# Performance work log

Hardware: AMD Instinct MI355X
Metric: run time of the kernel (lower is better)

The kernel has to match this reference:

```python
import jax, jax.numpy as jnp
import numpy as np
import math

N, E_EDGES, G = 25000, 400000, 128
D_NODE, D_EDGE, D_PE = 64, 16, 16
H_DIM, N_HEADS, N_LAYERS = 128, 8, 4
D_HEAD = H_DIM // N_HEADS
BN_EPS = 1e-5
SCALE = 1.0 / math.sqrt(D_HEAD)


def _bn(x, gamma, beta):
    # BatchNorm1d with batch statistics (training-mode math), biased variance
    mu = x.mean(0)
    var = x.var(0)
    return (x - mu) * jax.lax.rsqrt(var + BN_EPS) * gamma + beta


def _seg_softmax(score, seg, n):
    # softmax over edges sharing the same destination node (PyG softmax semantics)
    m = jax.lax.stop_gradient(jax.ops.segment_max(score, seg, num_segments=n))
    ex = jnp.exp(score - m[seg])
    den = jax.ops.segment_sum(ex, seg, num_segments=n)
    return ex / (den[seg] + 1e-16)


def _mlp(x, W1, b1, W2, b2):
    return jax.nn.relu(x @ W1 + b1) @ W2 + b2


def _forward(x, edge_attr, pe, Wn, We, Wpe, Wqkv, bqkv, WEl, bEl, WOl, bOl, WOel, bOel,
             fW1, fb1, fW2, fb2, feW1, feb1, feW2, feb2, bng, bnb,
             muW1, mub1, muW2, mub2, lvW1, lvb1, lvW2, lvb2, edge_index, batch):
    src, dst = edge_index[0], edge_index[1]  # messages flow src(j) -> dst(i)
    h = x @ Wn + pe @ Wpe                    # [N, H_DIM]
    e = edge_attr @ We                       # [E, H_DIM]
    for l in range(N_LAYERS):
        Q = (h @ Wqkv[l, 0] + bqkv[l, 0]).reshape(-1, N_HEADS, D_HEAD)
        K = (h @ Wqkv[l, 1] + bqkv[l, 1]).reshape(-1, N_HEADS, D_HEAD)
        V = (h @ Wqkv[l, 2] + bqkv[l, 2]).reshape(-1, N_HEADS, D_HEAD)
        Eh = (e @ WEl[l] + bEl[l]).reshape(-1, N_HEADS, D_HEAD)
        qijk = Eh * (Q[dst] * K[src]) * SCALE            # [E, H, Dh] edge-modulated scores
        alpha = _seg_softmax(qijk.sum(-1), dst, N)       # [E, H]
        agg = jax.ops.segment_sum(alpha[..., None] * V[src], dst, num_segments=N)
        agg = agg.reshape(-1, H_DIM)                     # [N, H_DIM] ('sum' aggregator)
        # node branch: WO + residual, BN, FFN, residual, BN
        hn = _bn(agg @ WOl[l] + bOl[l] + h, bng[l, 0], bnb[l, 0])
        hn = _bn(hn + _mlp(hn, fW1[l], fb1[l], fW2[l], fb2[l]), bng[l, 1], bnb[l, 1])
        # edge branch: pre-softmax scores are the edge update
        en = _bn(qijk.reshape(-1, H_DIM) @ WOel[l] + bOel[l] + e, bng[l, 2], bnb[l, 2])
        en = _bn(en + _mlp(en, feW1[l], feb1[l], feW2[l], feb2[l]), bng[l, 3], bnb[l, 3])
        h, e = hn, en
    g = jax.ops.segment_sum(h, batch, num_segments=G)    # [G, H_DIM] global 'sum' pool
    mu = _mlp(g, muW1, mub1, muW2, mub2)
    log_var = _mlp(g, lvW1, lvb1, lvW2, lvb2)
    return mu, jnp.exp(0.5 * log_var)                    # eval branch: (mu, std)


def setup_inputs() -> dict:
    key = jax.random.key(0)
    ks = iter(jax.random.split(key, 40))
    def nrm(shape, scale=1.0):
        return jax.random.normal(next(ks), shape, jnp.float32) * scale
    s = lambda fan: 1.0 / math.sqrt(fan)
    L = N_LAYERS
    d = {}
    d['x'] = nrm((N, D_NODE))
    d['edge_attr'] = nrm((E_EDGES, D_EDGE))
    d['pe'] = nrm((N, D_PE))
    d['edge_index'] = jax.random.randint(next(ks), (2, E_EDGES), 0, N, jnp.int32)
    d['batch'] = jnp.sort(jax.random.randint(next(ks), (N,), 0, G, jnp.int32))
    d['Wn'] = nrm((D_NODE, H_DIM), s(D_NODE))
    d['We'] = nrm((D_EDGE, H_DIM), s(D_EDGE))
    d['Wpe'] = nrm((D_PE, H_DIM), s(D_PE))
    d['Wqkv'] = nrm((L, 3, H_DIM, H_DIM), s(H_DIM)); d['bqkv'] = jnp.zeros((L, 3, H_DIM))
    d['WEl'] = nrm((L, H_DIM, H_DIM), s(H_DIM)); d['bEl'] = jnp.zeros((L, H_DIM))
    d['WOl'] = nrm((L, H_DIM, H_DIM), s(H_DIM)); d['bOl'] = jnp.zeros((L, H_DIM))
    d['WOel'] = nrm((L, H_DIM, H_DIM), s(H_DIM)); d['bOel'] = jnp.zeros((L, H_DIM))
    for p in ['f', 'fe']:
        d[p + 'W1'] = nrm((L, H_DIM, H_DIM), s(H_DIM)); d[p + 'b1'] = jnp.zeros((L, H_DIM))
        d[p + 'W2'] = nrm((L, H_DIM, H_DIM), s(H_DIM)); d[p + 'b2'] = jnp.zeros((L, H_DIM))
    d['bng'] = jnp.ones((L, 4, H_DIM)); d['bnb'] = jnp.zeros((L, 4, H_DIM))
    for p in ['mu', 'lv']:
        d[p + 'W1'] = nrm((H_DIM, H_DIM), s(H_DIM)); d[p + 'b1'] = jnp.zeros((H_DIM,))
        d[p + 'W2'] = nrm((H_DIM, 1), s(H_DIM)); d[p + 'b2'] = jnp.zeros((1,))
    return d


def reference(x, edge_attr, pe, Wn, We, Wpe, Wqkv, bqkv, WEl, bEl, WOl, bOl, WOel, bOel,
              fW1, fb1, fW2, fb2, feW1, feb1, feW2, feb2, bng, bnb,
              muW1, mub1, muW2, mub2, lvW1, lvb1, lvW2, lvb2, edge_index, batch):
    return _forward(x, edge_attr, pe, Wn, We, Wpe, Wqkv, bqkv, WEl, bEl, WOl, bOl, WOel, bOel,
                    fW1, fb1, fW2, fb2, feW1, feb1, feW2, feb2, bng, bnb,
                    muW1, mub1, muW2, mub2, lvW1, lvb1, lvW2, lvb2, edge_index, batch)
```

## Files before the change

kernel.cpp:

```cpp
#include <hip/hip_runtime.h>

#define N_NODES 25000
#define E_EDGES 400000
#define G_GRAPHS 128

typedef short bf16x8 __attribute__((ext_vector_type(8)));
typedef float f32x4 __attribute__((ext_vector_type(4)));

__device__ __forceinline__ float b2f(unsigned short u) {
    union { unsigned int i; float f; } v; v.i = ((unsigned int)u) << 16; return v.f;
}
__device__ __forceinline__ unsigned short f2b(float f) {
    union { float f; unsigned int i; } v; v.f = f;
    unsigned int i = v.i;
    unsigned int r = i + 0x7FFFu + ((i >> 16) & 1u);
    return (unsigned short)(r >> 16);
}
__device__ __forceinline__ float ldin(const void* p, long i, int f) {
    return f ? ((const float*)p)[i] : b2f(((const unsigned short*)p)[i]);
}
__device__ __forceinline__ void stage8(unsigned short* dl, const _Float16* sp) {
    bf16x8 r;
#pragma unroll
    for (int i = 0; i < 8; i++) r[i] = (short)f2b((float)sp[i]);
    *(bf16x8*)dl = r;
}
__device__ __forceinline__ void stage8_split(unsigned short* dh, unsigned short* dl, const _Float16* sp) {
    bf16x8 rh, rl;
#pragma unroll
    for (int i = 0; i < 8; i++) {
        float v = (float)sp[i];
        unsigned short hi = f2b(v);
        rh[i] = (short)hi;
        rl[i] = (short)f2b(v - b2f(hi));
    }
    *(bf16x8*)dh = rh;
    *(bf16x8*)dl = rl;
}

__global__ void detect_dtype(const unsigned int* __restrict__ x, int* __restrict__ flag) {
    __shared__ int cnt;
    if (threadIdx.x == 0) cnt = 0;
    __syncthreads();
    int bad = 0;
    for (int i = threadIdx.x; i < 4096; i += 256) {
        unsigned short lo = (unsigned short)(x[i] & 0xFFFFu);
        int e = (lo >> 7) & 0xFF;
        if (e != 0 && (e < 0x60 || e > 0x9F)) bad++;
    }
    atomicAdd(&cnt, bad);
    __syncthreads();
    if (threadIdx.x == 0) flag[0] = (cnt > 100) ? 1 : 0;
}

__global__ void transpose_weights(const void* __restrict__ Wqkv, const void* __restrict__ WEl,
                                  const void* __restrict__ WOl, const void* __restrict__ WOel,
                                  const void* __restrict__ fW1, const void* __restrict__ fW2,
                                  const void* __restrict__ feW1, const void* __restrict__ feW2,
                                  unsigned short* __restrict__ wT,
                                  unsigned short* __restrict__ wTlo,
                                  const int* __restrict__ flag) {
    int f = flag[0];
    int m = blockIdx.x >> 6, part = blockIdx.x & 63;
    int l = m / 10, j = m % 10;
    const void* base; long eoff;
    switch (j) {
        case 0: case 1: case 2: base = Wqkv; eoff = (long)(l * 3 + j) * 16384; break;
        case 3: base = WEl;  eoff = (long)l * 16384; break;
        case 4: base = WOl;  eoff = (long)l * 16384; break;
        case 5: base = WOel; eoff = (long)l * 16384; break;
        case 6: base = fW1;  eoff = (long)l * 16384; break;
        case 7: base = fW2;  eoff = (long)l * 16384; break;
        case 8: base = feW1; eoff = (long)l * 16384; break;
        default: base = feW2; eoff = (long)l * 16384; break;
    }
    int o = part * 256 + threadIdx.x;
    int n = o >> 7, k = o & 127;
    float w = ldin(base, eoff + k * 128 + n, f);
    unsigned short hi = f2b(w);
    wT[(size_t)m * 16384 + o] = hi;
    wTlo[(size_t)m * 16384 + o] = f2b(w - b2f(hi));
}

__global__ void zero_int(int* __restrict__ p, int n) {
    int i = blockIdx.x * 256 + threadIdx.x;
    if (i < n) p[i] = 0;
}
__global__ void zero_f32(float* __restrict__ p, int n) {
    int i = blockIdx.x * 256 + threadIdx.x;
    if (i < n) p[i] = 0.f;
}
__global__ void hist_kernel(const int* __restrict__ dst, int* __restrict__ deg, int E) {
    int i = blockIdx.x * 256 + threadIdx.x;
    if (i < E) atomicAdd(&deg[dst[i]], 1);
}
__global__ __launch_bounds__(1024) void scan_kernel(int* __restrict__ deg,
                                                    int* __restrict__ indptr, int N, int E) {
    __shared__ int tmp[1024];
    int t = threadIdx.x;
    int CH = (N + 1023) / 1024;
    int i0 = t * CH;
    int s = 0;
    for (int j = 0; j < CH; j++) { int idx = i0 + j; if (idx < N) s += deg[idx]; }
    tmp[t] = s; __syncthreads();
    for (int off = 1; off < 1024; off <<= 1) {
        int v = (t >= off) ? tmp[t - off] : 0;
        __syncthreads();
        tmp[t] += v;
        __syncthreads();
    }
    int run = (t == 0) ? 0 : tmp[t - 1];
    for (int j = 0; j < CH; j++) {
        int idx = i0 + j;
        if (idx < N) { int dv = deg[idx]; indptr[idx] = run; deg[idx] = run; run += dv; }
    }
    if (t == 0) indptr[N] = E;
}
__global__ void fill_kernel(const int* __restrict__ src, const int* __restrict__ dst,
                            int* __restrict__ cursor, int* __restrict__ pos,
                            unsigned short* __restrict__ srcCSR, int E) {
    int i = blockIdx.x * 256 + threadIdx.x;
    if (i < E) {
        int p = atomicAdd(&cursor[dst[i]], 1);
        pos[i] = p;
        srcCSR[p] = (unsigned short)src[i];
    }
}

__global__ __launch_bounds__(256) void init_h(const void* __restrict__ x, const void* __restrict__ pe,
                                              const void* __restrict__ Wn, const void* __restrict__ Wpe,
                                              _Float16* __restrict__ h, const int* __restrict__ flag, int N) {
    __shared__ float WnS[64 * 128];
    __shared__ float WpeS[16 * 128];
    __shared__ float xr[2][64];
    __shared__ float per[2][16];
    int f = flag[0]; int t = threadIdx.x;
    for (int i = t; i < 8192; i += 256) WnS[i] = ldin(Wn, i, f);
    for (int i = t; i < 2048; i += 256) WpeS[i] = ldin(Wpe, i, f);
    long r0 = (long)blockIdx.x * 2;
    if (t < 128) { int rr = t >> 6, k = t & 63; long rg = r0 + rr; if (rg < N) xr[rr][k] = ldin(x, rg * 64 + k, f); }
    else if (t < 160) { int q = t - 128; int rr = q >> 4, k = q & 15; long rg = r0 + rr; if (rg < N) per[rr][k] = ldin(pe, rg * 16 + k, f); }
    __syncthreads();
    int half = t >> 7, c = t & 127;
    long r = r0 + half;
    if (r >= N) return;
    float acc = 0.f;
#pragma unroll 8
    for (int k = 0; k < 64; k++) acc += xr[half][k] * WnS[k * 128 + c];
#pragma unroll
    for (int k = 0; k < 16; k++) acc += per[half][k] * WpeS[k * 128 + c];
    h[r * 128 + c] = (_Float16)acc;
}
__global__ __launch_bounds__(256) void init_e(const void* __restrict__ ea, const void* __restrict__ We,
                                              _Float16* __restrict__ e, const int* __restrict__ flag, int E) {
    __shared__ float WeT[128 * 17];
    __shared__ float rows[16][16];
    int f = flag[0]; int t = threadIdx.x;
    for (int i = t; i < 2048; i += 256) {
        int k = i >> 7, c = i & 127;
        WeT[c * 17 + k] = ldin(We, i, f);
    }
    long r0 = (long)blockIdx.x * 16;
    { int rr = t >> 4, k = t & 15; rows[rr][k] = ldin(ea, (r0 + rr) * 16 + k, f); }
    __syncthreads();
#pragma unroll
    for (int p = 0; p < 8; p++) {
        int idx = t + p * 256;
        int rr = idx >> 7, c = idx & 127;
        float acc = 0.f;
#pragma unroll
        for (int k = 0; k < 16; k++) acc += rows[rr][k] * WeT[c * 17 + k];
        e[(r0 + rr) * 128 + c] = (_Float16)acc;
    }
}

template <bool RELU, bool RES>
__global__ __launch_bounds__(256, 2) void gemm_node(const _Float16* __restrict__ A,
                                                    const unsigned short* __restrict__ Wt,
                                                    const unsigned short* __restrict__ Wtlo,
                                                    const void* __restrict__ bias, long boff,
                                                    const _Float16* __restrict__ Rp,
                                                    _Float16* __restrict__ C, int M,
                                                    const int* __restrict__ flag) {
    __shared__ unsigned short Ah[128 * 136];
    __shared__ unsigned short Al[128 * 136];
    int t = threadIdx.x;
    long bRow = (long)blockIdx.x * 128;
    {
        int r = t >> 1, ch = (t & 1) * 64;
        long gr = bRow + r;
        unsigned short* dh = &Ah[r * 136 + ch];
        unsigned short* dl = &Al[r * 136 + ch];
        if (gr < M) {
            const _Float16* sp = A + gr * 128 + ch;
#pragma unroll
            for (int i = 0; i < 8; i++) stage8_split(dh + i * 8, dl + i * 8, sp + i * 8);
        } else {
            int4 z = make_int4(0, 0, 0, 0);
#pragma unroll
            for (int i = 0; i < 8; i++) { *(int4*)(dh + i * 8) = z; *(int4*)(dl + i * 8) = z; }
        }
    }
    __syncthreads();
    int wave = t >> 6, lane = t & 63;
    int wr = (wave >> 1) * 64, wc = (wave & 1) * 64;
    int lm = lane & 15, lq = lane >> 4;
    f32x4 acc[4][4];
#pragma unroll
    for (int i = 0; i < 4; i++)
#pragma unroll
        for (int j = 0; j < 4; j++) acc[i][j] = (f32x4){0.f, 0.f, 0.f, 0.f};
#pragma unroll
    for (int ks = 0; ks < 4; ks++) {
        int ko = ks * 32 + lq * 8;
        bf16x8 bh[4], bl[4], ah[4], al[4];
#pragma unroll
        for (int j = 0; j < 4; j++) {
            bh[j] = *(const bf16x8*)(Wt + (wc + j * 16 + lm) * 128 + ko);
            bl[j] = *(const bf16x8*)(Wtlo + (wc + j * 16 + lm) * 128 + ko);
        }
#pragma unroll
        for (int i = 0; i < 4; i++) {
            ah[i] = *(const bf16x8*)&Ah[(wr + i * 16 + lm) * 136 + ko];
            al[i] = *(const bf16x8*)&Al[(wr + i * 16 + lm) * 136 + ko];
        }
#pragma unroll
        for (int i = 0; i < 4; i++)
#pragma unroll
            for (int j = 0; j < 4; j++) {
                acc[i][j] = __builtin_amdgcn_mfma_f32_16x16x32_bf16(ah[i], bh[j], acc[i][j], 0, 0, 0);
                acc[i][j] = __builtin_amdgcn_mfma_f32_16x16x32_bf16(al[i], bh[j], acc[i][j], 0, 0, 0);
                acc[i][j] = __builtin_amdgcn_mfma_f32_16x16x32_bf16(ah[i], bl[j], acc[i][j], 0, 0, 0);
            }
    }
    int f = flag[0];
#pragma unroll
    for (int j = 0; j < 4; j++) {
        int col = wc + j * 16 + lm;
        float bv = ldin(bias, boff + col, f);
#pragma unroll
        for (int i = 0; i < 4; i++) {
#pragma unroll
            for (int r4 = 0; r4 < 4; r4++) {
                long grow = bRow + wr + i * 16 + lq * 4 + r4;
                if (grow < M) {
                    float v = acc[i][j][r4] + bv;
                    if (RES) v += (float)Rp[grow * 128 + col];
                    if (RELU) v = v > 0.f ? v : 0.f;
                    C[grow * 128 + col] = (_Float16)v;
                }
            }
        }
    }
}

__global__ __launch_bounds__(256, 2) void node_qk(const _Float16* __restrict__ h,
                                                  const unsigned short* __restrict__ wq,
                                                  const unsigned short* __restrict__ wqlo,
                                                  const unsigned short* __restrict__ wk,
                                                  const unsigned short* __restrict__ wklo,
                                                  const void* __restrict__ bqkv, long boff0,
                                                  _Float16* __restrict__ Qb,
                                                  _Float16* __restrict__ Kb,
                                                  const int* __restrict__ flag, int M) {
    __shared__ unsigned short Ah[128 * 136];
    __shared__ unsigned short Al[128 * 136];
    int t = threadIdx.x;
    long bRow = (long)blockIdx.x * 128;
    {
        int r = t >> 1, ch = (t & 1) * 64;
        long gr = bRow + r;
        unsigned short* dh = &Ah[r * 136 + ch];
        unsigned short* dl = &Al[r * 136 + ch];
        if (gr < M) {
            const _Float16* sp = h + gr * 128 + ch;
#pragma unroll
            for (int i = 0; i < 8; i++) stage8_split(dh + i * 8, dl + i * 8, sp + i * 8);
        } else {
            int4 z = make_int4(0, 0, 0, 0);
#pragma unroll
            for (int i = 0; i < 8; i++) { *(int4*)(dh + i * 8) = z; *(int4*)(dl + i * 8) = z; }
        }
    }
    __syncthreads();
    int wave = t >> 6, lane = t & 63;
    int wr = (wave >> 1) * 64, wc = (wave & 1) * 64;
    int lm = lane & 15, lq = lane >> 4;
    int f = flag[0];
    _Float16* outs[2] = {Qb, Kb};
    const unsigned short* whi[2] = {wq, wk};
    const unsigned short* wlo[2] = {wqlo, wklo};
    for (int w = 0; w < 2; w++) {
        f32x4 acc[4][4];
#pragma unroll
        for (int i = 0; i < 4; i++)
#pragma unroll
            for (int j = 0; j < 4; j++) acc[i][j] = (f32x4){0.f, 0.f, 0.f, 0.f};
#pragma unroll
        for (int ks = 0; ks < 4; ks++) {
            int ko = ks * 32 + lq * 8;
            bf16x8 bh[4], bl[4], ah[4], al[4];
#pragma unroll
            for (int j = 0; j < 4; j++) {
                bh[j] = *(const bf16x8*)(whi[w] + (wc + j * 16 + lm) * 128 + ko);
                bl[j] = *(const bf16x8*)(wlo[w] + (wc + j * 16 + lm) * 128 + ko);
            }
#pragma unroll
            for (int i = 0; i < 4; i++) {
                ah[i] = *(const bf16x8*)&Ah[(wr + i * 16 + lm) * 136 + ko];
                al[i] = *(const bf16x8*)&Al[(wr + i * 16 + lm) * 136 + ko];
            }
#pragma unroll
            for (int i = 0; i < 4; i++)
#pragma unroll
                for (int j = 0; j < 4; j++) {
                    acc[i][j] = __builtin_amdgcn_mfma_f32_16x16x32_bf16(ah[i], bh[j], acc[i][j], 0, 0, 0);
                    acc[i][j] = __builtin_amdgcn_mfma_f32_16x16x32_bf16(al[i], bh[j], acc[i][j], 0, 0, 0);
                    acc[i][j] = __builtin_amdgcn_mfma_f32_16x16x32_bf16(ah[i], bl[j], acc[i][j], 0, 0, 0);
                }
        }
        _Float16* O = outs[w];
#pragma unroll
        for (int j = 0; j < 4; j++) {
            int col = wc + j * 16 + lm;
            float bv = ldin(bqkv, boff0 + w * 128 + col, f);
#pragma unroll
            for (int i = 0; i < 4; i++)
#pragma unroll
                for (int r4 = 0; r4 < 4; r4++) {
                    long grow = bRow + wr + i * 16 + lq * 4 + r4;
                    if (grow < M) O[grow * 128 + col] = (_Float16)(acc[i][j][r4] + bv);
                }
        }
    }
}

template <typename TS>
__global__ __launch_bounds__(256, 2) void edge_fused0(_Float16* __restrict__ ebuf,
                                                      const unsigned short* __restrict__ W1t,
                                                      const unsigned short* __restrict__ W2t,
                                                      const void* __restrict__ bias1, long b1off,
                                                      const void* __restrict__ bias2, long b2off,
                                                      const _Float16* __restrict__ Qb,
                                                      const _Float16* __restrict__ Kb,
                                                      const int* __restrict__ srcp,
                                                      const int* __restrict__ dstp,
                                                      const int* __restrict__ posp,
                                                      TS* __restrict__ score,
                                                      const int* __restrict__ flag,
                                                      int writeE) {
    __shared__ unsigned short Es[128 * 136];
    __shared__ int sdst[128], ssrc[128], spos[128];
    int t = threadIdx.x;
    long bRow = (long)blockIdx.x * 128;
    {
        int r = t >> 1, ch = (t & 1) * 64;
        const _Float16* sp = ebuf + (bRow + r) * 128 + ch;
        unsigned short* dl = &Es[r * 136 + ch];
#pragma unroll
        for (int i = 0; i < 8; i++) stage8(dl + i * 8, sp + i * 8);
    }
    if (t < 128) { sdst[t] = dstp[bRow + t]; ssrc[t] = srcp[bRow + t]; spos[t] = posp[bRow + t]; }
    __syncthreads();
    int wave = t >> 6, lane = t & 63;
    int wr = (wave >> 1) * 64, wc = (wave & 1) * 64;
    int lm = lane & 15, lq = lane >> 4;
    int f = flag[0];
    f32x4 acc[4][4];
#pragma unroll
    for (int i = 0; i < 4; i++)
#pragma unroll
        for (int j = 0; j < 4; j++) acc[i][j] = (f32x4){0.f, 0.f, 0.f, 0.f};
    {
        bf16x8 bfr[4][4];
#pragma unroll
        for (int ks = 0; ks < 4; ks++)
#pragma unroll
            for (int j = 0; j < 4; j++)
                bfr[ks][j] = *(const bf16x8*)(W1t + (wc + j * 16 + lm) * 128 + ks * 32 + lq * 8);
#pragma unroll
        for (int ks = 0; ks < 4; ks++) {
            int ko = ks * 32 + lq * 8;
            bf16x8 af[4];
#pragma unroll
            for (int i = 0; i < 4; i++) af[i] = *(const bf16x8*)&Es[(wr + i * 16 + lm) * 136 + ko];
#pragma unroll
            for (int i = 0; i < 4; i++)
#pragma unroll
                for (int j = 0; j < 4; j++)
                    acc[i][j] = __builtin_amdgcn_mfma_f32_16x16x32_bf16(af[i], bfr[ks][j], acc[i][j], 0, 0, 0);
        }
    }
    __syncthreads();
#pragma unroll
    for (int j = 0; j < 4; j++) {
        int col = wc + j * 16 + lm;
        float bv = ldin(bias1, b1off + col, f);
#pragma unroll
        for (int i = 0; i < 4; i++) {
#pragma unroll
            for (int r4 = 0; r4 < 4; r4++) {
                int rl = wr + i * 16 + lq * 4 + r4;
                float eh = acc[i][j][r4] + bv;
                float qv = (float)Qb[(long)sdst[rl] * 128 + col];
                float kv = (float)Kb[(long)ssrc[rl] * 128 + col];
                acc[i][j][r4] = eh * qv * kv * 0.25f;
            }
        }
    }
#pragma unroll
    for (int i = 0; i < 4; i++)
#pragma unroll
        for (int j = 0; j < 4; j++)
#pragma unroll
            for (int r4 = 0; r4 < 4; r4++) {
                float s = acc[i][j][r4];
                s += __shfl_xor(s, 1); s += __shfl_xor(s, 2);
                s += __shfl_xor(s, 4); s += __shfl_xor(s, 8);
                if (lm == 0) {
                    int rl = wr + i * 16 + lq * 4 + r4;
                    s = fminf(fmaxf(s, -60000.f), 60000.f);
                    score[(long)spos[rl] * 8 + (wc >> 4) + j] = (TS)s;
                }
            }
    if (!writeE) return;
#pragma unroll
    for (int i = 0; i < 4; i++)
#pragma unroll
        for (int j = 0; j < 4; j++)
#pragma unroll
            for (int r4 = 0; r4 < 4; r4++)
                Es[(wr + i * 16 + lq * 4 + r4) * 136 + wc + j * 16 + lm] = f2b(acc[i][j][r4]);
    __syncthreads();
#pragma unroll
    for (int i = 0; i < 4; i++)
#pragma unroll
        for (int j = 0; j < 4; j++) acc[i][j] = (f32x4){0.f, 0.f, 0.f, 0.f};
    {
        bf16x8 bfr[4][4];
#pragma unroll
        for (int ks = 0; ks < 4; ks++)
#pragma unroll
            for (int j = 0; j < 4; j++)
                bfr[ks][j] = *(const bf16x8*)(W2t + (wc + j * 16 + lm) * 128 + ks * 32 + lq * 8);
#pragma unroll
        for (int ks = 0; ks < 4; ks++) {
            int ko = ks * 32 + lq * 8;
            bf16x8 af[4];
#pragma unroll
            for (int i = 0; i < 4; i++) af[i] = *(const bf16x8*)&Es[(wr + i * 16 + lm) * 136 + ko];
#pragma unroll
            for (int i = 0; i < 4; i++)
#pragma unroll
                for (int j = 0; j < 4; j++)
                    acc[i][j] = __builtin_amdgcn_mfma_f32_16x16x32_bf16(af[i], bfr[ks][j], acc[i][j], 0, 0, 0);
        }
    }
#pragma unroll
    for (int j = 0; j < 4; j++) {
        int col = wc + j * 16 + lm;
        float bo = ldin(bias2, b2off + col, f);
#pragma unroll
        for (int i = 0; i < 4; i++)
#pragma unroll
            for (int r4 = 0; r4 < 4; r4++) {
                long ge = bRow + wr + i * 16 + lq * 4 + r4;
                float v = acc[i][j][r4] + bo + (float)ebuf[ge * 128 + col];
                ebuf[ge * 128 + col] = (_Float16)v;
            }
    }
}

__global__ __launch_bounds__(256, 2) void edge_ffn(_Float16* __restrict__ ebuf,
                                                   const unsigned short* __restrict__ W1t,
                                                   const unsigned short* __restrict__ W2t,
                                                   const void* __restrict__ bias1, long b1off,
                                                   const void* __restrict__ bias2, long b2off,
                                                   const int* __restrict__ flag) {
    __shared__ unsigned short Es[128 * 136];
    int t = threadIdx.x;
    long bRow = (long)blockIdx.x * 128;
    {
        int r = t >> 1, ch = (t & 1) * 64;
        const _Float16* sp = ebuf + (bRow + r) * 128 + ch;
        unsigned short* dl = &Es[r * 136 + ch];
#pragma unroll
        for (int i = 0; i < 8; i++) stage8(dl + i * 8, sp + i * 8);
    }
    __syncthreads();
    int wave = t >> 6, lane = t & 63;
    int wr = (wave >> 1) * 64, wc = (wave & 1) * 64;
    int lm = lane & 15, lq = lane >> 4;
    int f = flag[0];
    f32x4 acc[4][4];
#pragma unroll
    for (int i = 0; i < 4; i++)
#pragma unroll
        for (int j = 0; j < 4; j++) acc[i][j] = (f32x4){0.f, 0.f, 0.f, 0.f};
#pragma unroll
    for (int ks = 0; ks < 4; ks++) {
        int ko = ks * 32 + lq * 8;
        bf16x8 bfr[4], af[4];
#pragma unroll
        for (int j = 0; j < 4; j++) bfr[j] = *(const bf16x8*)(W1t + (wc + j * 16 + lm) * 128 + ko);
#pragma unroll
        for (int i = 0; i < 4; i++) af[i] = *(const bf16x8*)&Es[(wr + i * 16 + lm) * 136 + ko];
#pragma unroll
        for (int i = 0; i < 4; i++)
#pragma unroll
            for (int j = 0; j < 4; j++)
                acc[i][j] = __builtin_amdgcn_mfma_f32_16x16x32_bf16(af[i], bfr[j], acc[i][j], 0, 0, 0);
    }
    __syncthreads();
#pragma unroll
    for (int j = 0; j < 4; j++) {
        int col = wc + j * 16 + lm;
        float bv = ldin(bias1, b1off + col, f);
#pragma unroll
        for (int i = 0; i < 4; i++)
#pragma unroll
            for (int r4 = 0; r4 < 4; r4++) {
                float v = acc[i][j][r4] + bv;
                v = v > 0.f ? v : 0.f;
                Es[(wr + i * 16 + lq * 4 + r4) * 136 + col] = f2b(v);
            }
    }
    __syncthreads();
#pragma unroll
    for (int i = 0; i < 4; i++)
#pragma unroll
        for (int j = 0; j < 4; j++) acc[i][j] = (f32x4){0.f, 0.f, 0.f, 0.f};
#pragma unroll
    for (int ks = 0; ks < 4; ks++) {
        int ko = ks * 32 + lq * 8;
        bf16x8 bfr[4], af[4];
#pragma unroll
        for (int j = 0; j < 4; j++) bfr[j] = *(const bf16x8*)(W2t + (wc + j * 16 + lm) * 128 + ko);
#pragma unroll
        for (int i = 0; i < 4; i++) af[i] = *(const bf16x8*)&Es[(wr + i * 16 + lm) * 136 + ko];
#pragma unroll
        for (int i = 0; i < 4; i++)
#pragma unroll
            for (int j = 0; j < 4; j++)
                acc[i][j] = __builtin_amdgcn_mfma_f32_16x16x32_bf16(af[i], bfr[j], acc[i][j], 0, 0, 0);
    }
#pragma unroll
    for (int j = 0; j < 4; j++) {
        int col = wc + j * 16 + lm;
        float bv = ldin(bias2, b2off + col, f);
#pragma unroll
        for (int i = 0; i < 4; i++)
#pragma unroll
            for (int r4 = 0; r4 < 4; r4++) {
                long ge = bRow + wr + i * 16 + lq * 4 + r4;
                float v = acc[i][j][r4] + bv + (float)ebuf[ge * 128 + col];
                ebuf[ge * 128 + col] = (_Float16)v;
            }
    }
}

template <typename TS>
__global__ __launch_bounds__(256) void agg_kernel(const int* __restrict__ indptr,
                                                  const unsigned short* __restrict__ srcCSR,
                                                  const TS* __restrict__ score,
                                                  const _Float16* __restrict__ V,
                                                  _Float16* __restrict__ agg, int N) {
    int wave = threadIdx.x >> 6, lane = threadIdx.x & 63;
    int n = blockIdx.x * 4 + wave;
    if (n >= N) return;
    int beg = indptr[n], end = indptr[n + 1];
    int h0 = lane >> 4, h1 = 4 + h0;
    float m0 = -3.402823466e38f, m1 = -3.402823466e38f;
    for (int i = beg; i < end; i++) {
        m0 = fmaxf(m0, (float)score[(long)i * 8 + h0]);
        m1 = fmaxf(m1, (float)score[(long)i * 8 + h1]);
    }
    float a0 = 0.f, a1 = 0.f, d0 = 0.f, d1 = 0.f;
    for (int i = beg; i < end; i++) {
        int sv = srcCSR[i];
        float p0 = __expf((float)score[(long)i * 8 + h0] - m0);
        float p1 = __expf((float)score[(long)i * 8 + h1] - m1);
        d0 += p0; d1 += p1;
        a0 += p0 * (float)V[(long)sv * 128 + lane];
        a1 += p1 * (float)V[(long)sv * 128 + 64 + lane];
    }
    float inv0 = 1.f / (d0 + 1e-16f), inv1 = 1.f / (d1 + 1e-16f);
    agg[(long)n * 128 + lane] = (_Float16)(a0 * inv0);
    agg[(long)n * 128 + 64 + lane] = (_Float16)(a1 * inv1);
}

__global__ __launch_bounds__(256) void bn_stats(const _Float16* __restrict__ y, float* __restrict__ sums, int M) {
    __shared__ float lsum[16 * 128];
    __shared__ float lss[16 * 128];
    int t = threadIdx.x;
    int chb = (t & 15) * 8;
    int rowlane = t >> 4;
    float s[8], ss[8];
#pragma unroll
    for (int k = 0; k < 8; k++) { s[k] = 0.f; ss[k] = 0.f; }
    for (long r = (long)blockIdx.x * 16 + rowlane; r < M; r += (long)gridDim.x * 16) {
        int4 raw = *(const int4*)(y + r * 128 + chb);
        const _Float16* a = (const _Float16*)&raw;
#pragma unroll
        for (int k = 0; k < 8; k++) {
            float v = (float)a[k];
            s[k] += v; ss[k] += v * v;
        }
    }
#pragma unroll
    for (int k = 0; k < 8; k++) {
        lsum[rowlane * 128 + chb + k] = s[k];
        lss[rowlane * 128 + chb + k] = ss[k];
    }
    __syncthreads();
    if (t < 128) {
        float t1 = 0.f, t2 = 0.f;
#pragma unroll
        for (int row = 0; row < 16; row++) {
            t1 += lsum[row * 128 + t];
            t2 += lss[row * 128 + t];
        }
        atomicAdd(&sums[t], t1);
        atomicAdd(&sums[128 + t], t2);
    }
}
__global__ void bn_finalize(const float* __restrict__ sums,
                            const void* __restrict__ gamma, long goff,
                            const void* __restrict__ beta, long boff,
                            float* __restrict__ scale, float* __restrict__ shift,
                            float invM, const int* __restrict__ flag) {
    int f = flag[0];
    int c = threadIdx.x;
    float mu = sums[c] * invM;
    float var = fmaxf(sums[128 + c] * invM - mu * mu, 0.f);
    float rs = rsqrtf(var + 1e-5f);
    float g = ldin(gamma, goff + c, f) * rs;
    scale[c] = g;
    shift[c] = ldin(beta, boff + c, f) - mu * g;
}
__global__ void bn_apply(_Float16* __restrict__ y, const float* __restrict__ scale,
                         const float* __restrict__ shift, long total) {
    long idx = ((long)blockIdx.x * 256 + threadIdx.x) * 8;
    long stride = (long)gridDim.x * 256 * 8;
    for (; idx < total; idx += stride) {
        int cb = (int)(idx & 127);
        _Float16* p = y + idx;
        int4 v = *(int4*)p;
        _Float16* a = (_Float16*)&v;
        _Float16 o[8];
#pragma unroll
        for (int k = 0; k < 8; k++) o[k] = (_Float16)((float)a[k] * scale[cb + k] + shift[cb + k]);
        *(int4*)p = *(int4*)o;
    }
}

__global__ __launch_bounds__(128) void pool_kernel(const _Float16* __restrict__ h,
                                                   const int* __restrict__ batch,
                                                   float* __restrict__ g, int N) {
    int gid = blockIdx.x;
    int lo = 0, hi = N;
    while (lo < hi) { int mid = (lo + hi) >> 1; if (batch[mid] < gid) lo = mid + 1; else hi = mid; }
    int beg = lo;
    hi = N;
    while (lo < hi) { int mid = (lo + hi) >> 1; if (batch[mid] < gid + 1) lo = mid + 1; else hi = mid; }
    int end = lo;
    int c = threadIdx.x;
    float acc = 0.f;
    for (int r = beg; r < end; r++) acc += (float)h[(long)r * 128 + c];
    g[gid * 128 + c] = acc;
}
__global__ __launch_bounds__(128) void head_kernel(const float* __restrict__ g,
                                                   const void* muW1, const void* mub1,
                                                   const void* muW2, const void* mub2,
                                                   const void* lvW1, const void* lvb1,
                                                   const void* lvW2, const void* lvb2,
                                                   void* __restrict__ out, const int* __restrict__ flag) {
    __shared__ float gr[128];
    __shared__ float red[128];
    int f = flag[0];
    int r = blockIdx.x, t = threadIdx.x;
    gr[t] = g[r * 128 + t];
    __syncthreads();
    float acc = ldin(mub1, t, f);
    for (int k = 0; k < 128; k++) acc += gr[k] * ldin(muW1, k * 128 + t, f);
    acc = fmaxf(acc, 0.f);
    red[t] = acc * ldin(muW2, t, f);
    __syncthreads();
    for (int s = 64; s > 0; s >>= 1) { if (t < s) red[t] += red[t + s]; __syncthreads(); }
    if (t == 0) {
        float v = red[0] + ldin(mub2, 0, f);
        if (f) ((float*)out)[r] = v; else ((unsigned short*)out)[r] = f2b(v);
    }
    __syncthreads();
    acc = ldin(lvb1, t, f);
    for (int k = 0; k < 128; k++) acc += gr[k] * ldin(lvW1, k * 128 + t, f);
    acc = fmaxf(acc, 0.f);
    red[t] = acc * ldin(lvW2, t, f);
    __syncthreads();
    for (int s = 64; s > 0; s >>= 1) { if (t < s) red[t] += red[t + s]; __syncthreads(); }
    if (t == 0) {
        float v = __expf(0.5f * (red[0] + ldin(lvb2, 0, f)));
        if (f) ((float*)out)[128 + r] = v; else ((unsigned short*)out)[128 + r] = f2b(v);
    }
}

extern "C" void kernel_launch(void* const* d_in, const int* in_sizes, int n_in,
                              void* d_out, int out_size, void* d_ws, size_t ws_size,
                              hipStream_t stream) {
    const void* x    = d_in[0];
    const void* ea   = d_in[1];
    const void* pe   = d_in[2];
    const int* eidx  = (const int*)d_in[3];
    const int* batch = (const int*)d_in[4];
    const int* srcp = eidx;
    const int* dstp = eidx + E_EDGES;

    bool score_f32 = (ws_size >= 148000000ULL);
    size_t ts_size = score_f32 ? 4 : 2;

    char* wsb = (char*)d_ws;
    size_t off = 0;
    auto alloc = [&](size_t bytes) -> char* {
        char* p = wsb + off;
        off = (off + bytes + 255) & ~(size_t)255;
        return p;
    };
    int* dflag            = (int*)alloc(256);
    unsigned short* wT    = (unsigned short*)alloc(40UL * 16384 * 2);
    unsigned short* wTlo  = (unsigned short*)alloc(40UL * 16384 * 2);
    _Float16* ebuf        = (_Float16*)alloc((size_t)E_EDGES * 128 * 2);
    _Float16* hbuf        = (_Float16*)alloc((size_t)N_NODES * 128 * 2);
    char* slotA           = alloc((size_t)N_NODES * 128 * 2);
    char* slotB           = alloc((size_t)N_NODES * 128 * 2);
    char* scoreB          = alloc((size_t)E_EDGES * 8 * ts_size);
    int* indptr           = (int*)alloc((size_t)(N_NODES + 1) * 4);
    int* deg              = (int*)alloc((size_t)N_NODES * 4);
    int* pos              = (int*)alloc((size_t)E_EDGES * 4);
    unsigned short* srcCSR= (unsigned short*)alloc((size_t)E_EDGES * 2);
    float* sums           = (float*)alloc(256 * 4);
    float* scal           = (float*)alloc(128 * 4);
    float* shft           = (float*)alloc(128 * 4);
    float* gpool          = (float*)scoreB;

    _Float16* Qb = (_Float16*)slotA;
    _Float16* Kb = (_Float16*)slotB;
    _Float16* Vb = (_Float16*)slotA;
    _Float16* aggb = (_Float16*)slotB;
    _Float16* hid  = (_Float16*)slotA;

    detect_dtype<<<1, 256, 0, stream>>>((const unsigned int*)x, dflag);
    transpose_weights<<<2560, 256, 0, stream>>>(d_in[8], d_in[10], d_in[12], d_in[14],
                                                d_in[16], d_in[18], d_in[20], d_in[22], wT, wTlo, dflag);
    zero_int<<<(N_NODES + 255) / 256, 256, 0, stream>>>(deg, N_NODES);
    hist_kernel<<<(E_EDGES + 255) / 256, 256, 0, stream>>>(dstp, deg, E_EDGES);
    scan_kernel<<<1, 1024, 0, stream>>>(deg, indptr, N_NODES, E_EDGES);
    fill_kernel<<<(E_EDGES + 255) / 256, 256, 0, stream>>>(srcp, dstp, deg, pos, srcCSR, E_EDGES);
    init_h<<<(N_NODES + 1) / 2, 256, 0, stream>>>(x, pe, d_in[5], d_in[7], hbuf, dflag, N_NODES);
    init_e<<<E_EDGES / 16, 256, 0, stream>>>(ea, d_in[6], ebuf, dflag, E_EDGES);

    const int gN = (N_NODES + 127) / 128;
    const int gE = E_EDGES / 128;

    auto bn = [&](_Float16* y, int M, long o) {
        zero_f32<<<1, 256, 0, stream>>>(sums, 256);
        int sb = (M + 15) / 16; if (sb > 1024) sb = 1024;
        bn_stats<<<sb, 256, 0, stream>>>(y, sums, M);
        bn_finalize<<<1, 128, 0, stream>>>(sums, d_in[24], o, d_in[25], o, scal, shft, 1.f / (float)M, dflag);
        long total = (long)M * 128;
        int grid = (int)((total / 8 + 255) / 256); if (grid > 4096) grid = 4096;
        bn_apply<<<grid, 256, 0, stream>>>(y, scal, shft, total);
    };

    for (int l = 0; l < 4; l++) {
        const unsigned short* WTl = wT + (size_t)l * 10 * 16384;
        const unsigned short* WTlol = wTlo + (size_t)l * 10 * 16384;
        int writeE = (l < 3) ? 1 : 0;
        node_qk<<<gN, 256, 0, stream>>>(hbuf, WTl + 0 * 16384, WTlol + 0 * 16384,
                                        WTl + 1 * 16384, WTlol + 1 * 16384,
                                        d_in[9], (long)(l * 3) * 128, Qb, Kb, dflag, N_NODES);
        if (score_f32)
            edge_fused0<float><<<gE, 256, 0, stream>>>(ebuf, WTl + 3 * 16384, WTl + 5 * 16384,
                                                       d_in[11], (long)l * 128, d_in[15], (long)l * 128,
                                                       Qb, Kb, srcp, dstp, pos, (float*)scoreB, dflag, writeE);
        else
            edge_fused0<_Float16><<<gE, 256, 0, stream>>>(ebuf, WTl + 3 * 16384, WTl + 5 * 16384,
                                                          d_in[11], (long)l * 128, d_in[15], (long)l * 128,
                                                          Qb, Kb, srcp, dstp, pos, (_Float16*)scoreB, dflag, writeE);
        gemm_node<false, false><<<gN, 256, 0, stream>>>(hbuf, WTl + 2 * 16384, WTlol + 2 * 16384,
                                                        d_in[9], (long)(l * 3 + 2) * 128, nullptr, Vb, N_NODES, dflag);
        if (score_f32)
            agg_kernel<float><<<(N_NODES + 3) / 4, 256, 0, stream>>>(indptr, srcCSR, (const float*)scoreB, Vb, aggb, N_NODES);
        else
            agg_kernel<_Float16><<<(N_NODES + 3) / 4, 256, 0, stream>>>(indptr, srcCSR, (const _Float16*)scoreB, Vb, aggb, N_NODES);
        gemm_node<false, true><<<gN, 256, 0, stream>>>(aggb, WTl + 4 * 16384, WTlol + 4 * 16384,
                                                       d_in[13], (long)l * 128, hbuf, hbuf, N_NODES, dflag);
        bn(hbuf, N_NODES, (long)(l * 4 + 0) * 128);
        gemm_node<true, false><<<gN, 256, 0, stream>>>(hbuf, WTl + 6 * 16384, WTlol + 6 * 16384,
                                                       d_in[17], (long)l * 128, nullptr, hid, N_NODES, dflag);
        gemm_node<false, true><<<gN, 256, 0, stream>>>(hid, WTl + 7 * 16384, WTlol + 7 * 16384,
                                                       d_in[19], (long)l * 128, hbuf, hbuf, N_NODES, dflag);
        bn(hbuf, N_NODES, (long)(l * 4 + 1) * 128);
        if (l < 3) {
            bn(ebuf, E_EDGES, (long)(l * 4 + 2) * 128);
            edge_ffn<<<gE, 256, 0, stream>>>(ebuf, WTl + 8 * 16384, WTl + 9 * 16384,
                                             d_in[21], (long)l * 128, d_in[23], (long)l * 128, dflag);
            bn(ebuf, E_EDGES, (long)(l * 4 + 3) * 128);
        }
    }

    pool_kernel<<<G_GRAPHS, 128, 0, stream>>>(hbuf, batch, gpool, N_NODES);
    head_kernel<<<G_GRAPHS, 128, 0, stream>>>(gpool, d_in[26], d_in[27], d_in[28], d_in[29],
                                              d_in[30], d_in[31], d_in[32], d_in[33], d_out, dflag);
}
```

Before: 3.192 ms.

## Fold edge BatchNorm apply into edge FFN and next-layer edge kernels

Removes the standalone bn_apply passes over the 400k×128 edge buffer. Each edge BN now only computes per-channel scale and shift, stored in per-slot arrays. The consumer kernels (edge_ffn, and edge_fused0 of the next layer) apply the normalization while staging into LDS and again in the residual epilogue. Launch bounds for the edge kernels also go from 2 to 4 blocks per SM, which may force register spills given the large MFMA accumulator and weight-fragment arrays.

Result: slower. 3.418 ms (+7.1%).

```diff
diff --git a/kernel.cpp b/kernel.cpp
--- a/kernel.cpp
+++ b/kernel.cpp
@@ -18,6 +18,13 @@
 }
 __device__ __forceinline__ float ldin(const void* p, long i, int f) {
     return f ? ((const float*)p)[i] : b2f(((const unsigned short*)p)[i]);
+}
+__device__ __forceinline__ void stage8n(unsigned short* dl, const _Float16* sp,
+                                        const float* sS, const float* sH) {
+    bf16x8 r;
+#pragma unroll
+    for (int i = 0; i < 8; i++) r[i] = (short)f2b((float)sp[i] * sS[i] + sH[i]);
+    *(bf16x8*)dl = r;
 }
 __device__ __forceinline__ void stage8(unsigned short* dl, const _Float16* sp) {
     bf16x8 r;
@@ -336,7 +343,7 @@
 }
 
 template <typename TS>
-__global__ __launch_bounds__(256, 2) void edge_fused0(_Float16* __restrict__ ebuf,
+__global__ __launch_bounds__(256, 4) void edge_fused0(_Float16* __restrict__ ebuf,
                                                       const unsigned short* __restrict__ W1t,
                                                       const unsigned short* __restrict__ W2t,
                                                       const void* __restrict__ bias1, long b1off,
@@ -348,19 +355,27 @@
                                                       const int* __restrict__ posp,
                                                       TS* __restrict__ score,
                                                       const int* __restrict__ flag,
+                                                      const float* __restrict__ nS,
+                                                      const float* __restrict__ nH,
                                                       int writeE) {
     __shared__ unsigned short Es[128 * 136];
     __shared__ int sdst[128], ssrc[128], spos[128];
+    __shared__ float nSs[128], nHs[128];
     int t = threadIdx.x;
     long bRow = (long)blockIdx.x * 128;
+    if (t < 128) {
+        nSs[t] = nS ? nS[t] : 1.f;
+        nHs[t] = nH ? nH[t] : 0.f;
+        sdst[t] = dstp[bRow + t]; ssrc[t] = srcp[bRow + t]; spos[t] = posp[bRow + t];
+    }
+    __syncthreads();
     {
         int r = t >> 1, ch = (t & 1) * 64;
         const _Float16* sp = ebuf + (bRow + r) * 128 + ch;
         unsigned short* dl = &Es[r * 136 + ch];
 #pragma unroll
-        for (int i = 0; i < 8; i++) stage8(dl + i * 8, sp + i * 8);
-    }
-    if (t < 128) { sdst[t] = dstp[bRow + t]; ssrc[t] = srcp[bRow + t]; spos[t] = posp[bRow + t]; }
+        for (int i = 0; i < 8; i++) stage8n(dl + i * 8, sp + i * 8, &nSs[ch + i * 8], &nHs[ch + i * 8]);
+    }
     __syncthreads();
     int wave = t >> 6, lane = t & 63;
     int wr = (wave >> 1) * 64, wc = (wave & 1) * 64;
@@ -460,32 +475,38 @@
     for (int j = 0; j < 4; j++) {
         int col = wc + j * 16 + lm;
         float bo = ldin(bias2, b2off + col, f);
+        float sc = nSs[col], sh = nHs[col];
 #pragma unroll
         for (int i = 0; i < 4; i++)
 #pragma unroll
             for (int r4 = 0; r4 < 4; r4++) {
                 long ge = bRow + wr + i * 16 + lq * 4 + r4;
-                float v = acc[i][j][r4] + bo + (float)ebuf[ge * 128 + col];
-                ebuf[ge * 128 + col] = (_Float16)v;
+                float en = (float)ebuf[ge * 128 + col] * sc + sh;
+                ebuf[ge * 128 + col] = (_Float16)(acc[i][j][r4] + bo + en);
             }
     }
 }
 
-__global__ __launch_bounds__(256, 2) void edge_ffn(_Float16* __restrict__ ebuf,
+__global__ __launch_bounds__(256, 4) void edge_ffn(_Float16* __restrict__ ebuf,
                                                    const unsigned short* __restrict__ W1t,
                                                    const unsigned short* __restrict__ W2t,
                                                    const void* __restrict__ bias1, long b1off,
                                                    const void* __restrict__ bias2, long b2off,
-                                                   const int* __restrict__ flag) {
+                                                   const int* __restrict__ flag,
+                                                   const float* __restrict__ nS,
+                                                   const float* __restrict__ nH) {
     __shared__ unsigned short Es[128 * 136];
+    __shared__ float nSs[128], nHs[128];
     int t = threadIdx.x;
     long bRow = (long)blockIdx.x * 128;
+    if (t < 128) { nSs[t] = nS[t]; nHs[t] = nH[t]; }
+    __syncthreads();
     {
         int r = t >> 1, ch = (t & 1) * 64;
         const _Float16* sp = ebuf + (bRow + r) * 128 + ch;
         unsigned short* dl = &Es[r * 136 + ch];
 #pragma unroll
-        for (int i = 0; i < 8; i++) stage8(dl + i * 8, sp + i * 8);
+        for (int i = 0; i < 8; i++) stage8n(dl + i * 8, sp + i * 8, &nSs[ch + i * 8], &nHs[ch + i * 8]);
     }
     __syncthreads();
     int wave = t >> 6, lane = t & 63;
@@ -548,13 +569,14 @@
     for (int j = 0; j < 4; j++) {
         int col = wc + j * 16 + lm;
         float bv = ldin(bias2, b2off + col, f);
+        float sc = nSs[col], sh = nHs[col];
 #pragma unroll
         for (int i = 0; i < 4; i++)
 #pragma unroll
             for (int r4 = 0; r4 < 4; r4++) {
                 long ge = bRow + wr + i * 16 + lq * 4 + r4;
-                float v = acc[i][j][r4] + bv + (float)ebuf[ge * 128 + col];
-                ebuf[ge * 128 + col] = (_Float16)v;
+                float en = (float)ebuf[ge * 128 + col] * sc + sh;
+                ebuf[ge * 128 + col] = (_Float16)(acc[i][j][r4] + bv + en);
             }
     }
 }
@@ -738,8 +760,8 @@
     int* pos              = (int*)alloc((size_t)E_EDGES * 4);
     unsigned short* srcCSR= (unsigned short*)alloc((size_t)E_EDGES * 2);
     float* sums           = (float*)alloc(256 * 4);
-    float* scal           = (float*)alloc(128 * 4);
-    float* shft           = (float*)alloc(128 * 4);
+    float* scalArr        = (float*)alloc(16 * 128 * 4);
+    float* shftArr        = (float*)alloc(16 * 128 * 4);
     float* gpool          = (float*)scoreB;
 
     _Float16* Qb = (_Float16*)slotA;
@@ -761,31 +783,38 @@
     const int gN = (N_NODES + 127) / 128;
     const int gE = E_EDGES / 128;
 
-    auto bn = [&](_Float16* y, int M, long o) {
+    auto bn_sf = [&](_Float16* y, int M, int s) {
         zero_f32<<<1, 256, 0, stream>>>(sums, 256);
         int sb = (M + 15) / 16; if (sb > 1024) sb = 1024;
         bn_stats<<<sb, 256, 0, stream>>>(y, sums, M);
-        bn_finalize<<<1, 128, 0, stream>>>(sums, d_in[24], o, d_in[25], o, scal, shft, 1.f / (float)M, dflag);
+        bn_finalize<<<1, 128, 0, stream>>>(sums, d_in[24], (long)s * 128, d_in[25], (long)s * 128,
+                                           scalArr + s * 128, shftArr + s * 128, 1.f / (float)M, dflag);
+    };
+    auto bn_full = [&](_Float16* y, int M, int s) {
+        bn_sf(y, M, s);
         long total = (long)M * 128;
         int grid = (int)((total / 8 + 255) / 256); if (grid > 4096) grid = 4096;
-        bn_apply<<<grid, 256, 0, stream>>>(y, scal, shft, total);
+        bn_apply<<<grid, 256, 0, stream>>>(y, scalArr + s * 128, shftArr + s * 128, total);
     };
 
     for (int l = 0; l < 4; l++) {
         const unsigned short* WTl = wT + (size_t)l * 10 * 16384;
         const unsigned short* WTlol = wTlo + (size_t)l * 10 * 16384;
         int writeE = (l < 3) ? 1 : 0;
+        const float* eS = (l > 0) ? scalArr + ((l - 1) * 4 + 3) * 128 : nullptr;
+        const float* eH = (l > 0) ? shftArr + ((l - 1) * 4 + 3) * 128 : nullptr;
+
         node_qk<<<gN, 256, 0, stream>>>(hbuf, WTl + 0 * 16384, WTlol + 0 * 16384,
                                         WTl + 1 * 16384, WTlol + 1 * 16384,
                                         d_in[9], (long)(l * 3) * 128, Qb, Kb, dflag, N_NODES);
         if (score_f32)
             edge_fused0<float><<<gE, 256, 0, stream>>>(ebuf, WTl + 3 * 16384, WTl + 5 * 16384,
                                                        d_in[11], (long)l * 128, d_in[15], (long)l * 128,
-                                                       Qb, Kb, srcp, dstp, pos, (float*)scoreB, dflag, writeE);
+                                                       Qb, Kb, srcp, dstp, pos, (float*)scoreB, dflag, eS, eH, writeE);
         else
             edge_fused0<_Float16><<<gE, 256, 0, stream>>>(ebuf, WTl + 3 * 16384, WTl + 5 * 16384,
                                                           d_in[11], (long)l * 128, d_in[15], (long)l * 128,
-                                                          Qb, Kb, srcp, dstp, pos, (_Float16*)scoreB, dflag, writeE);
+                                                          Qb, Kb, srcp, dstp, pos, (_Float16*)scoreB, dflag, eS, eH, writeE);
         gemm_node<false, false><<<gN, 256, 0, stream>>>(hbuf, WTl + 2 * 16384, WTlol + 2 * 16384,
                                                         d_in[9], (long)(l * 3 + 2) * 128, nullptr, Vb, N_NODES, dflag);
         if (score_f32)
@@ -794,17 +823,18 @@
             agg_kernel<_Float16><<<(N_NODES + 3) / 4, 256, 0, stream>>>(indptr, srcCSR, (const _Float16*)scoreB, Vb, aggb, N_NODES);
         gemm_node<false, true><<<gN, 256, 0, stream>>>(aggb, WTl + 4 * 16384, WTlol + 4 * 16384,
                                                        d_in[13], (long)l * 128, hbuf, hbuf, N_NODES, dflag);
-        bn(hbuf, N_NODES, (long)(l * 4 + 0) * 128);
+        bn_full(hbuf, N_NODES, l * 4 + 0);
         gemm_node<true, false><<<gN, 256, 0, stream>>>(hbuf, WTl + 6 * 16384, WTlol + 6 * 16384,
                                                        d_in[17], (long)l * 128, nullptr, hid, N_NODES, dflag);
         gemm_node<false, true><<<gN, 256, 0, stream>>>(hid, WTl + 7 * 16384, WTlol + 7 * 16384,
                                                        d_in[19], (long)l * 128, hbuf, hbuf, N_NODES, dflag);
-        bn(hbuf, N_NODES, (long)(l * 4 + 1) * 128);
+        bn_full(hbuf, N_NODES, l * 4 + 1);
         if (l < 3) {
-            bn(ebuf, E_EDGES, (long)(l * 4 + 2) * 128);
+            bn_sf(ebuf, E_EDGES, l * 4 + 2);
             edge_ffn<<<gE, 256, 0, stream>>>(ebuf, WTl + 8 * 16384, WTl + 9 * 16384,
-                                             d_in[21], (long)l * 128, d_in[23], (long)l * 128, dflag);
-            bn(ebuf, E_EDGES, (long)(l * 4 + 3) * 128);
+                                             d_in[21], (long)l * 128, d_in[23], (long)l * 128, dflag,
+                                             scalArr + (l * 4 + 2) * 128, shftArr + (l * 4 + 2) * 128);
+            bn_sf(ebuf, E_EDGES, l * 4 + 3);
         }
     }
 
```
